# Kernel optimization log

Measured on AMD Instinct MI355X. Metric: run time of the kernel, lower is better.

Reference implementation:

```python
import jax, jax.numpy as jnp
import numpy as np
import math

D_MODEL = 2048
D_QK = 128
D_V = 128
SEQ = 4096

def setup_inputs() -> dict:
    key = jax.random.key(0)
    ks = jax.random.split(key, 9)
    s = 1.0 / math.sqrt(D_MODEL)
    return {
        "input_q": jax.random.normal(ks[0], (SEQ, D_MODEL), jnp.float32),
        "input_k": jax.random.normal(ks[1], (SEQ, D_MODEL), jnp.float32),
        "input_v": jax.random.normal(ks[2], (SEQ, D_MODEL), jnp.float32),
        "WQ_w": jax.random.normal(ks[3], (D_QK, D_MODEL), jnp.float32) * s,
        "WQ_b": jax.random.normal(ks[4], (D_QK,), jnp.float32) * s,
        "WK_w": jax.random.normal(ks[5], (D_QK, D_MODEL), jnp.float32) * s,
        "WK_b": jax.random.normal(ks[6], (D_QK,), jnp.float32) * s,
        "WV_w": jax.random.normal(ks[7], (D_V, D_MODEL), jnp.float32) * s,
        "WV_b": jax.random.normal(ks[8], (D_V,), jnp.float32) * s,
    }

def reference(input_q, input_k, input_v, WQ_w, WQ_b, WK_w, WK_b, WV_w, WV_b):
    # Linear projections (torch nn.Linear: x @ W.T + b)
    Q = input_q @ WQ_w.T + WQ_b   # [S, d_qk]
    K = input_k @ WK_w.T + WK_b   # [S, d_qk]
    V = input_v @ WV_w.T + WV_b   # [S, d_v]
    S = Q.shape[0]
    # causal mask: -inf strictly above the diagonal, 0 elsewhere
    mask = jnp.triu(jnp.full((S, S), -jnp.inf, dtype=Q.dtype), k=1)
    # NOTE: original code adds mask BEFORE dividing by sqrt(d_model)
    scores = (Q @ K.T + mask) / math.sqrt(D_MODEL)  # [S, S]
    attn = jax.nn.softmax(scores, axis=-1)
    return attn @ V  # [S, d_v]
```

## Files before the change

kernel.cpp:

```cpp
#include <hip/hip_runtime.h>

#define SEQ 4096
#define DM  2048
#define DH  128
#define NSPLIT 8

typedef __attribute__((ext_vector_type(8))) short bf16x8;
typedef __attribute__((ext_vector_type(4))) short short4v;
typedef __attribute__((ext_vector_type(4))) float f32x4;

__device__ inline short f2bf(float f) {
    union { float f; unsigned u; } x; x.f = f;
    unsigned r = x.u + 0x7fffu + ((x.u >> 16) & 1u);
    return (short)(r >> 16);
}

__device__ inline float fexp2(float f) { return __builtin_amdgcn_exp2f(f); }

__device__ inline void lds_barrier() {
    asm volatile("s_waitcnt lgkmcnt(0)\n\ts_barrier" ::: "memory");
}

__global__ __launch_bounds__(256) void convw_kernel(
    const float* __restrict__ wq, const float* __restrict__ wk, const float* __restrict__ wv,
    short* __restrict__ Wbf)
{
    int idx = blockIdx.x * 256 + threadIdx.x;
    int mat = idx >> 16;
    int off = (idx & 65535) * 4;
    const float* W = (mat == 0) ? wq : (mat == 1) ? wk : wv;
    float4 v = *reinterpret_cast<const float4*>(W + off);
    short4v s = { f2bf(v.x), f2bf(v.y), f2bf(v.z), f2bf(v.w) };
    *reinterpret_cast<short4v*>(Wbf + (size_t)mat * DH * DM + off) = s;
}

__global__ __launch_bounds__(256) void proj_kernel(
    const float* __restrict__ inq, const float* __restrict__ ink, const float* __restrict__ inv,
    const short* __restrict__ Wbf,
    const float* __restrict__ bq, const float* __restrict__ bk, const float* __restrict__ bv,
    short* __restrict__ Qws, short* __restrict__ Kws, short* __restrict__ Vtws)
{
    const int mat = blockIdx.y;
    const float* A    = (mat == 0) ? inq : (mat == 1) ? ink : inv;
    const float* bias = (mat == 0) ? bq  : (mat == 1) ? bk  : bv;

    const int tid  = threadIdx.x;
    const int lane = tid & 63;
    const int w    = tid >> 6;
    const int g    = lane >> 4;
    const int c16  = lane & 15;
    const int i0   = blockIdx.x * 32;

    __shared__ short Alds[32][72];
    __shared__ short Wlds[128][72];

    const int ar = tid >> 3, ac = (tid & 7) * 8;
    const float* Aload = A + (size_t)(i0 + ar) * DM + ac;
    const int wr = tid >> 1, wc = (tid & 1) * 32;
    const short* Wload = Wbf + (size_t)mat * DH * DM + (size_t)wr * DM + wc;

    f32x4 acc[2][2];
    #pragma unroll
    for (int mI = 0; mI < 2; mI++)
        #pragma unroll
        for (int n = 0; n < 2; n++) acc[mI][n] = (f32x4){0.f, 0.f, 0.f, 0.f};

    float4  abuf[4][2];
    bf16x8  wbuf[2][4];

    #pragma unroll
    for (int d = 0; d < 2; d++)
        #pragma unroll
        for (int j = 0; j < 4; j++)
            wbuf[d][j] = *reinterpret_cast<const bf16x8*>(Wload + d * 64 + j * 8);
    #pragma unroll
    for (int d = 0; d < 4; d++)
        #pragma unroll
        for (int j = 0; j < 2; j++)
            abuf[d][j] = *reinterpret_cast<const float4*>(Aload + d * 64 + j * 4);

    #pragma unroll
    for (int c = 0; c < 32; c++) {
        const int da = c & 3, dw = c & 1;
        {
            #pragma unroll
            for (int j = 0; j < 4; j++)
                *reinterpret_cast<bf16x8*>(&Wlds[wr][wc + j * 8]) = wbuf[dw][j];
            float4 v0 = abuf[da][0], v1 = abuf[da][1];
            bf16x8 sv = { f2bf(v0.x), f2bf(v0.y), f2bf(v0.z), f2bf(v0.w),
                          f2bf(v1.x), f2bf(v1.y), f2bf(v1.z), f2bf(v1.w) };
            *reinterpret_cast<bf16x8*>(&Alds[ar][ac]) = sv;
        }
        if (c + 2 < 32) {
            #pragma unroll
            for (int j = 0; j < 4; j++)
                wbuf[dw][j] = *reinterpret_cast<const bf16x8*>(Wload + (c + 2) * 64 + j * 8);
        }
        if (c + 4 < 32) {
            #pragma unroll
            for (int j = 0; j < 2; j++)
                abuf[da][j] = *reinterpret_cast<const float4*>(Aload + (c + 4) * 64 + j * 4);
        }
        lds_barrier();
        #pragma unroll
        for (int kk = 0; kk < 2; kk++) {
            bf16x8 af0 = *reinterpret_cast<const bf16x8*>(&Alds[c16][kk * 32 + g * 8]);
            bf16x8 af1 = *reinterpret_cast<const bf16x8*>(&Alds[16 + c16][kk * 32 + g * 8]);
            #pragma unroll
            for (int n = 0; n < 2; n++) {
                bf16x8 wf = *reinterpret_cast<const bf16x8*>(
                    &Wlds[w * 32 + n * 16 + c16][kk * 32 + g * 8]);
                acc[0][n] = __builtin_amdgcn_mfma_f32_16x16x32_bf16(af0, wf, acc[0][n], 0, 0, 0);
                acc[1][n] = __builtin_amdgcn_mfma_f32_16x16x32_bf16(af1, wf, acc[1][n], 0, 0, 0);
            }
        }
        lds_barrier();
    }

    if (mat < 2) {
        short* outp = (mat == 0) ? Qws : Kws;
        #pragma unroll
        for (int mI = 0; mI < 2; mI++) {
            int row0 = i0 + mI * 16 + g * 4;
            #pragma unroll
            for (int n = 0; n < 2; n++) {
                int col = w * 32 + n * 16 + c16;
                float b = bias[col];
                #pragma unroll
                for (int r = 0; r < 4; r++)
                    outp[(size_t)(row0 + r) * DH + col] = f2bf(acc[mI][n][r] + b);
            }
        }
    } else {
        #pragma unroll
        for (int mI = 0; mI < 2; mI++) {
            int row0 = i0 + mI * 16 + g * 4;
            #pragma unroll
            for (int n = 0; n < 2; n++) {
                int col = w * 32 + n * 16 + c16;
                float b = bias[col];
                short4v o = { f2bf(acc[mI][n][0] + b), f2bf(acc[mI][n][1] + b),
                              f2bf(acc[mI][n][2] + b), f2bf(acc[mI][n][3] + b) };
                *reinterpret_cast<short4v*>(Vtws + (size_t)col * SEQ + row0) = o;
            }
        }
    }
}

__global__ __launch_bounds__(256) void flash_kernel(
    const short* __restrict__ Qws, const short* __restrict__ Kws, const short* __restrict__ Vtws,
    float* __restrict__ Opart, float* __restrict__ mpart, float* __restrict__ lpart)
{
    const int qb = blockIdx.x;
    const int y  = blockIdx.y;
    const int tid = threadIdx.x;
    const int w    = tid >> 6;
    const int lane = tid & 63;
    const int g = lane >> 4, c16 = lane & 15;
    const int i0 = qb * 64 + w * 16;

    __shared__ short Klds[64][136];
    __shared__ short Vlds[128][72];
    __shared__ short Slds[4][16][72];

    const int kkey = tid >> 2,  kdim = (tid & 3) * 32;
    const int vdim = tid >> 1,  vkey = (tid & 1) * 32;

    bf16x8 kreg[4], vreg[4];

    bf16x8 qf[4];
    #pragma unroll
    for (int kk = 0; kk < 4; kk++)
        qf[kk] = *reinterpret_cast<const bf16x8*>(Qws + (size_t)(i0 + c16) * DH + kk * 32 + g * 8);

    float m[4], lsum[4];
    f32x4 O[8];
    #pragma unroll
    for (int r = 0; r < 4; r++) { m[r] = -__builtin_inff(); lsum[r] = 0.f; }
    #pragma unroll
    for (int c = 0; c < 8; c++) O[c] = (f32x4){0.f, 0.f, 0.f, 0.f};

    const float C = 0.03188448666f;

    if (qb >= y) {
        {
            const int j0 = y * 64;
            #pragma unroll
            for (int j = 0; j < 4; j++) {
                kreg[j] = *reinterpret_cast<const bf16x8*>(
                    Kws + (size_t)(j0 + kkey) * DH + kdim + j * 8);
                vreg[j] = *reinterpret_cast<const bf16x8*>(
                    Vtws + (size_t)vdim * SEQ + j0 + vkey + j * 8);
            }
            #pragma unroll
            for (int j = 0; j < 4; j++) {
                *reinterpret_cast<bf16x8*>(&Klds[kkey][kdim + j * 8]) = kreg[j];
                *reinterpret_cast<bf16x8*>(&Vlds[vdim][vkey + j * 8]) = vreg[j];
            }
        }
        lds_barrier();

        for (int jt = y; jt <= qb; jt += NSPLIT) {
            const bool more = (jt + NSPLIT <= qb);
            if (more) {
                const int jn = (jt + NSPLIT) * 64;
                #pragma unroll
                for (int j = 0; j < 4; j++) {
                    kreg[j] = *reinterpret_cast<const bf16x8*>(
                        Kws + (size_t)(jn + kkey) * DH + kdim + j * 8);
                    vreg[j] = *reinterpret_cast<const bf16x8*>(
                        Vtws + (size_t)vdim * SEQ + jn + vkey + j * 8);
                }
            }
            const int j0 = jt * 64;
            f32x4 S[4];
            #pragma unroll
            for (int t = 0; t < 4; t++) S[t] = (f32x4){0.f, 0.f, 0.f, 0.f};
            #pragma unroll
            for (int kk = 0; kk < 4; kk++) {
                #pragma unroll
                for (int t = 0; t < 4; t++) {
                    bf16x8 kf = *reinterpret_cast<const bf16x8*>(
                        &Klds[t * 16 + c16][kk * 32 + g * 8]);
                    S[t] = __builtin_amdgcn_mfma_f32_16x16x32_bf16(qf[kk], kf, S[t], 0, 0, 0);
                }
            }
            float s2[4][4];
            #pragma unroll
            for (int t = 0; t < 4; t++) {
                int key = j0 + t * 16 + c16;
                #pragma unroll
                for (int r = 0; r < 4; r++) {
                    int q = i0 + g * 4 + r;
                    s2[t][r] = (key > q) ? -__builtin_inff() : S[t][r] * C;
                }
            }
            float mnew[4], alpha[4];
            #pragma unroll
            for (int r = 0; r < 4; r++) {
                float rm = fmaxf(fmaxf(s2[0][r], s2[1][r]), fmaxf(s2[2][r], s2[3][r]));
                rm = fmaxf(rm, __shfl_xor(rm, 1));
                rm = fmaxf(rm, __shfl_xor(rm, 2));
                rm = fmaxf(rm, __shfl_xor(rm, 4));
                rm = fmaxf(rm, __shfl_xor(rm, 8));
                mnew[r] = fmaxf(m[r], rm);
                alpha[r] = fexp2(m[r] - mnew[r]);
                m[r] = mnew[r];
            }
            #pragma unroll
            for (int r = 0; r < 4; r++) {
                float ps = 0.f;
                #pragma unroll
                for (int t = 0; t < 4; t++) {
                    float p = fexp2(s2[t][r] - mnew[r]);
                    ps += p;
                    Slds[w][g * 4 + r][t * 16 + c16] = f2bf(p);
                }
                ps += __shfl_xor(ps, 1);
                ps += __shfl_xor(ps, 2);
                ps += __shfl_xor(ps, 4);
                ps += __shfl_xor(ps, 8);
                lsum[r] = lsum[r] * alpha[r] + ps;
                #pragma unroll
                for (int c = 0; c < 8; c++) O[c][r] *= alpha[r];
            }
            #pragma unroll
            for (int kk2 = 0; kk2 < 2; kk2++) {
                bf16x8 pf = *reinterpret_cast<const bf16x8*>(&Slds[w][c16][kk2 * 32 + g * 8]);
                #pragma unroll
                for (int c = 0; c < 8; c++) {
                    bf16x8 vf = *reinterpret_cast<const bf16x8*>(
                        &Vlds[c * 16 + c16][kk2 * 32 + g * 8]);
                    O[c] = __builtin_amdgcn_mfma_f32_16x16x32_bf16(pf, vf, O[c], 0, 0, 0);
                }
            }
            lds_barrier();
            if (more) {
                #pragma unroll
                for (int j = 0; j < 4; j++) {
                    *reinterpret_cast<bf16x8*>(&Klds[kkey][kdim + j * 8]) = kreg[j];
                    *reinterpret_cast<bf16x8*>(&Vlds[vdim][vkey + j * 8]) = vreg[j];
                }
                lds_barrier();
            }
        }
        #pragma unroll
        for (int c = 0; c < 8; c++) {
            int col = c * 16 + c16;
            #pragma unroll
            for (int r = 0; r < 4; r++)
                Opart[((size_t)y * SEQ + i0 + g * 4 + r) * DH + col] = O[c][r];
        }
    }
    if (c16 == 0) {
        #pragma unroll
        for (int r = 0; r < 4; r++) {
            mpart[y * SEQ + i0 + g * 4 + r] = m[r];
            lpart[y * SEQ + i0 + g * 4 + r] = lsum[r];
        }
    }
}

__global__ __launch_bounds__(256) void merge_kernel(
    const float* __restrict__ Opart, const float* __restrict__ mpart, const float* __restrict__ lpart,
    float* __restrict__ out, int NS)
{
    const int row = blockIdx.x * 2 + (threadIdx.x >> 7);
    const int col = threadIdx.x & 127;
    float mh[16];
    float M = -__builtin_inff();
    for (int hh = 0; hh < NS; hh++) {
        mh[hh] = mpart[hh * SEQ + row];
        M = fmaxf(M, mh[hh]);
    }
    float denom = 0.f, num = 0.f;
    for (int hh = 0; hh < NS; hh++) {
        float wgt = fexp2(mh[hh] - M);
        denom += lpart[hh * SEQ + row] * wgt;
        num   += Opart[((size_t)hh * SEQ + row) * DH + col] * wgt;
    }
    out[(size_t)row * DH + col] = num / denom;
}

extern "C" void kernel_launch(void* const* d_in, const int* in_sizes, int n_in,
                              void* d_out, int out_size, void* d_ws, size_t ws_size,
                              hipStream_t stream) {
    const float* inq = (const float*)d_in[0];
    const float* ink = (const float*)d_in[1];
    const float* inv = (const float*)d_in[2];
    const float* wq  = (const float*)d_in[3];
    const float* bq  = (const float*)d_in[4];
    const float* wk  = (const float*)d_in[5];
    const float* bk  = (const float*)d_in[6];
    const float* wv  = (const float*)d_in[7];
    const float* bv  = (const float*)d_in[8];

    char* ws = (char*)d_ws;
    short* Qws   = (short*)(ws);
    short* Kws   = (short*)(ws + (1u << 20));
    short* Vtws  = (short*)(ws + (2u << 20));
    short* Wbf   = (short*)(ws + (3u << 20));
    float* Opart = (float*)(ws + 4718592);
    float* mpart = (float*)(ws + 4718592 + (size_t)NSPLIT * SEQ * DH * 4);
    float* lpart = mpart + (size_t)NSPLIT * SEQ;

    convw_kernel<<<768, 256, 0, stream>>>(wq, wk, wv, Wbf);
    proj_kernel<<<dim3(128, 3), 256, 0, stream>>>(inq, ink, inv, Wbf, bq, bk, bv, Qws, Kws, Vtws);
    flash_kernel<<<dim3(64, NSPLIT), 256, 0, stream>>>(Qws, Kws, Vtws, Opart, mpart, lpart);
    merge_kernel<<<2048, 256, 0, stream>>>(Opart, mpart, lpart, (float*)d_out, NSPLIT);
}
```

Before: 189.2 us.

## Restructure projection GEMM: smaller row tiles, W fragments from global, double-buffered LDS

The projection kernel now handles 16 rows per block instead of 32, doubling the grid to 768 blocks so more CUs stay busy. Weight fragments are loaded straight from global memory into registers in MFMA layout instead of being staged through LDS. The A tile is double-buffered in LDS so each step needs one barrier rather than two. The cost is that each weight element is reused across fewer rows, so global/L2 traffic for W rises, and a launch-bounds hint of 4 blocks per CU is added.

```diff
diff --git a/kernel.cpp b/kernel.cpp
--- a/kernel.cpp
+++ b/kernel.cpp
@@ -34,7 +34,7 @@
     *reinterpret_cast<short4v*>(Wbf + (size_t)mat * DH * DM + off) = s;
 }
 
-__global__ __launch_bounds__(256) void proj_kernel(
+__global__ __launch_bounds__(256, 4) void proj_kernel(
     const float* __restrict__ inq, const float* __restrict__ ink, const float* __restrict__ inv,
     const short* __restrict__ Wbf,
     const float* __restrict__ bq, const float* __restrict__ bk, const float* __restrict__ bv,
@@ -49,100 +49,92 @@
     const int w    = tid >> 6;
     const int g    = lane >> 4;
     const int c16  = lane & 15;
-    const int i0   = blockIdx.x * 32;
-
-    __shared__ short Alds[32][72];
-    __shared__ short Wlds[128][72];
-
-    const int ar = tid >> 3, ac = (tid & 7) * 8;
+    const int i0   = blockIdx.x * 16;
+
+    __shared__ short Alds[2][16][72];
+
+    const int ar = tid >> 4, ac = (tid & 15) * 4;
     const float* Aload = A + (size_t)(i0 + ar) * DM + ac;
-    const int wr = tid >> 1, wc = (tid & 1) * 32;
-    const short* Wload = Wbf + (size_t)mat * DH * DM + (size_t)wr * DM + wc;
-
-    f32x4 acc[2][2];
-    #pragma unroll
-    for (int mI = 0; mI < 2; mI++)
-        #pragma unroll
-        for (int n = 0; n < 2; n++) acc[mI][n] = (f32x4){0.f, 0.f, 0.f, 0.f};
-
-    float4  abuf[4][2];
-    bf16x8  wbuf[2][4];
-
+
+    const short* Wbase = Wbf + (size_t)mat * DH * DM + (size_t)(w * 32 + c16) * DM + g * 8;
+
+    f32x4 acc[2];
+    acc[0] = (f32x4){0.f, 0.f, 0.f, 0.f};
+    acc[1] = (f32x4){0.f, 0.f, 0.f, 0.f};
+
+    float4  abuf[4];
+    bf16x8  wfrag[2][4];
+
+    #pragma unroll
+    for (int d = 0; d < 4; d++)
+        abuf[d] = *reinterpret_cast<const float4*>(Aload + d * 64);
     #pragma unroll
     for (int d = 0; d < 2; d++)
         #pragma unroll
-        for (int j = 0; j < 4; j++)
-            wbuf[d][j] = *reinterpret_cast<const bf16x8*>(Wload + d * 64 + j * 8);
-    #pragma unroll
-    for (int d = 0; d < 4; d++)
-        #pragma unroll
-        for (int j = 0; j < 2; j++)
-            abuf[d][j] = *reinterpret_cast<const float4*>(Aload + d * 64 + j * 4);
+        for (int n = 0; n < 2; n++)
+            #pragma unroll
+            for (int kk = 0; kk < 2; kk++)
+                wfrag[d][n * 2 + kk] = *reinterpret_cast<const bf16x8*>(
+                    Wbase + (size_t)n * 16 * DM + d * 64 + kk * 32);
+
+    {
+        float4 v = abuf[0];
+        short4v sv = { f2bf(v.x), f2bf(v.y), f2bf(v.z), f2bf(v.w) };
+        *reinterpret_cast<short4v*>(&Alds[0][ar][ac]) = sv;
+        abuf[0] = *reinterpret_cast<const float4*>(Aload + 4 * 64);
+    }
+    lds_barrier();
 
     #pragma unroll
     for (int c = 0; c < 32; c++) {
-        const int da = c & 3, dw = c & 1;
-        {
-            #pragma unroll
-            for (int j = 0; j < 4; j++)
-                *reinterpret_cast<bf16x8*>(&Wlds[wr][wc + j * 8]) = wbuf[dw][j];
-            float4 v0 = abuf[da][0], v1 = abuf[da][1];
-            bf16x8 sv = { f2bf(v0.x), f2bf(v0.y), f2bf(v0.z), f2bf(v0.w),
-                          f2bf(v1.x), f2bf(v1.y), f2bf(v1.z), f2bf(v1.w) };
-            *reinterpret_cast<bf16x8*>(&Alds[ar][ac]) = sv;
-        }
+        if (c + 1 < 32) {
+            float4 v = abuf[(c + 1) & 3];
+            short4v sv = { f2bf(v.x), f2bf(v.y), f2bf(v.z), f2bf(v.w) };
+            *reinterpret_cast<short4v*>(&Alds[(c + 1) & 1][ar][ac]) = sv;
+        }
+        if (c + 5 < 32)
+            abuf[(c + 1) & 3] = *reinterpret_cast<const float4*>(Aload + (c + 5) * 64);
+
+        #pragma unroll
+        for (int kk = 0; kk < 2; kk++) {
+            bf16x8 af = *reinterpret_cast<const bf16x8*>(&Alds[c & 1][c16][kk * 32 + g * 8]);
+            #pragma unroll
+            for (int n = 0; n < 2; n++)
+                acc[n] = __builtin_amdgcn_mfma_f32_16x16x32_bf16(
+                    af, wfrag[c & 1][n * 2 + kk], acc[n], 0, 0, 0);
+        }
+
         if (c + 2 < 32) {
             #pragma unroll
-            for (int j = 0; j < 4; j++)
-                wbuf[dw][j] = *reinterpret_cast<const bf16x8*>(Wload + (c + 2) * 64 + j * 8);
-        }
-        if (c + 4 < 32) {
-            #pragma unroll
-            for (int j = 0; j < 2; j++)
-                abuf[da][j] = *reinterpret_cast<const float4*>(Aload + (c + 4) * 64 + j * 4);
-        }
-        lds_barrier();
-        #pragma unroll
-        for (int kk = 0; kk < 2; kk++) {
-            bf16x8 af0 = *reinterpret_cast<const bf16x8*>(&Alds[c16][kk * 32 + g * 8]);
-            bf16x8 af1 = *reinterpret_cast<const bf16x8*>(&Alds[16 + c16][kk * 32 + g * 8]);
-            #pragma unroll
-            for (int n = 0; n < 2; n++) {
-                bf16x8 wf = *reinterpret_cast<const bf16x8*>(
-                    &Wlds[w * 32 + n * 16 + c16][kk * 32 + g * 8]);
-                acc[0][n] = __builtin_amdgcn_mfma_f32_16x16x32_bf16(af0, wf, acc[0][n], 0, 0, 0);
-                acc[1][n] = __builtin_amdgcn_mfma_f32_16x16x32_bf16(af1, wf, acc[1][n], 0, 0, 0);
-            }
-        }
-        lds_barrier();
-    }
-
+            for (int n = 0; n < 2; n++)
+                #pragma unroll
+                for (int kk = 0; kk < 2; kk++)
+                    wfrag[c & 1][n * 2 + kk] = *reinterpret_cast<const bf16x8*>(
+                        Wbase + (size_t)n * 16 * DM + (c + 2) * 64 + kk * 32);
+        }
+
+        if (c + 1 < 32) lds_barrier();
+    }
+
+    const int row0 = i0 + g * 4;
     if (mat < 2) {
         short* outp = (mat == 0) ? Qws : Kws;
         #pragma unroll
-        for (int mI = 0; mI < 2; mI++) {
-            int row0 = i0 + mI * 16 + g * 4;
-            #pragma unroll
-            for (int n = 0; n < 2; n++) {
-                int col = w * 32 + n * 16 + c16;
-                float b = bias[col];
-                #pragma unroll
-                for (int r = 0; r < 4; r++)
-                    outp[(size_t)(row0 + r) * DH + col] = f2bf(acc[mI][n][r] + b);
-            }
+        for (int n = 0; n < 2; n++) {
+            int col = w * 32 + n * 16 + c16;
+            float b = bias[col];
+            #pragma unroll
+            for (int r = 0; r < 4; r++)
+                outp[(size_t)(row0 + r) * DH + col] = f2bf(acc[n][r] + b);
         }
     } else {
         #pragma unroll
-        for (int mI = 0; mI < 2; mI++) {
-            int row0 = i0 + mI * 16 + g * 4;
-            #pragma unroll
-            for (int n = 0; n < 2; n++) {
-                int col = w * 32 + n * 16 + c16;
-                float b = bias[col];
-                short4v o = { f2bf(acc[mI][n][0] + b), f2bf(acc[mI][n][1] + b),
-                              f2bf(acc[mI][n][2] + b), f2bf(acc[mI][n][3] + b) };
-                *reinterpret_cast<short4v*>(Vtws + (size_t)col * SEQ + row0) = o;
-            }
+        for (int n = 0; n < 2; n++) {
+            int col = w * 32 + n * 16 + c16;
+            float b = bias[col];
+            short4v o = { f2bf(acc[n][0] + b), f2bf(acc[n][1] + b),
+                          f2bf(acc[n][2] + b), f2bf(acc[n][3] + b) };
+            *reinterpret_cast<short4v*>(Vtws + (size_t)col * SEQ + row0) = o;
         }
     }
 }
@@ -345,7 +337,7 @@
     float* lpart = mpart + (size_t)NSPLIT * SEQ;
 
     convw_kernel<<<768, 256, 0, stream>>>(wq, wk, wv, Wbf);
-    proj_kernel<<<dim3(128, 3), 256, 0, stream>>>(inq, ink, inv, Wbf, bq, bk, bv, Qws, Kws, Vtws);
+    proj_kernel<<<dim3(256, 3), 256, 0, stream>>>(inq, ink, inv, Wbf, bq, bk, bv, Qws, Kws, Vtws);
     flash_kernel<<<dim3(64, NSPLIT), 256, 0, stream>>>(Qws, Kws, Vtws, Opart, mpart, lpart);
     merge_kernel<<<2048, 256, 0, stream>>>(Opart, mpart, lpart, (float*)d_out, NSPLIT);
 }
```

New measurement: 205.3 us. 8.5% more time.
